# Performance work log

Measured on AMD Instinct MI355X. Metric: run time of the kernel, lower is better.

## Reference

```python
import jax, jax.numpy as jnp
import numpy as np

NUM_IMAGES = 2
A = 96000              # Hi*Wi*num_anchors for one feature level
PRE_NMS_TOPK = 1000
POST_NMS_TOPK = 500
NMS_THRESH = 0.7
MIN_SIZE = 0.0
CLIP_ANGLE_THRESH = 1.0     # detectron2 RotatedBoxes.clip default
IMG_H, IMG_W = 320.0, 320.0
MAXV = 8                     # max #vertices of a rect-rect intersection polygon


def _cross(u, v):
    return u[..., 0] * v[..., 1] - u[..., 1] * v[..., 0]


def _box_corners(box):
    # box: [5] = (cx, cy, w, h, angle_deg) -> [4,2] CCW corners
    cx, cy, w, h, ang = box[0], box[1], box[2], box[3], box[4]
    t = ang * (jnp.pi / 180.0)
    c, s = jnp.cos(t), jnp.sin(t)
    dx = jnp.array([0.5, -0.5, -0.5, 0.5], box.dtype) * w
    dy = jnp.array([0.5, 0.5, -0.5, -0.5], box.dtype) * h
    return jnp.stack([cx + c * dx - s * dy, cy + s * dx + c * dy], axis=-1)


def _clip_halfplane(pts, n, a, b):
    # Sutherland-Hodgman clip of convex polygon pts[:n] against directed line a->b
    idx = jnp.arange(MAXV)
    valid = idx < n
    nxt = pts[jnp.where(idx + 1 < n, idx + 1, 0)]
    d_cur = _cross(b - a, pts - a)
    d_nxt = _cross(b - a, nxt - a)
    in_cur = d_cur >= 0
    in_nxt = d_nxt >= 0
    denom = d_cur - d_nxt
    denom = jnp.where(jnp.abs(denom) < 1e-12, 1e-12, denom)
    t = (d_cur / denom)[:, None]
    inter = pts + t * (nxt - pts)
    emit_cur = valid & in_cur
    emit_int = valid & (in_cur != in_nxt)
    cand = jnp.stack([pts, inter], axis=1).reshape(2 * MAXV, 2)
    emit = jnp.stack([emit_cur, emit_int], axis=1).reshape(2 * MAXV)
    pos = jnp.cumsum(emit) - 1
    dst = jnp.where(emit, pos, MAXV)  # out-of-range -> dropped
    out = jnp.zeros((MAXV, 2), pts.dtype).at[dst].set(cand, mode='drop')
    return out, emit.sum()


def _pair_iou(b1, b2):
    # exact rotated-box IoU (polygon intersection), matches pairwise_iou_rotated math
    p = jnp.zeros((MAXV, 2), b1.dtype).at[:4].set(_box_corners(b1))
    n = jnp.asarray(4)
    c2 = _box_corners(b2)
    for i in range(4):
        p, n = _clip_halfplane(p, n, c2[i], c2[(i + 1) % 4])
    idx = jnp.arange(MAXV)
    valid = idx < n
    nxt = p[jnp.where(idx + 1 < n, idx + 1, 0)]
    inter = 0.5 * jnp.abs(jnp.sum(jnp.where(valid, _cross(p, nxt), 0.0)))
    a1 = b1[2] * b1[3]
    a2 = b2[2] * b2[3]
    return inter / jnp.maximum(a1 + a2 - inter, 1e-12)


_iou_matrix = jax.vmap(jax.vmap(_pair_iou, (None, 0)), (0, None))


def _clip_boxes(b):
    # RotatedBoxes.clip: only boxes with |angle| <= 1 deg are axis-aligned clipped
    cx, cy, w, h, a = b[:, 0], b[:, 1], b[:, 2], b[:, 3], b[:, 4]
    x1 = jnp.clip(cx - w * 0.5, 0.0, IMG_W)
    y1 = jnp.clip(cy - h * 0.5, 0.0, IMG_H)
    x2 = jnp.clip(cx + w * 0.5, 0.0, IMG_W)
    y2 = jnp.clip(cy + h * 0.5, 0.0, IMG_H)
    near0 = jnp.abs(a) <= CLIP_ANGLE_THRESH
    ncx = jnp.where(near0, 0.5 * (x1 + x2), cx)
    ncy = jnp.where(near0, 0.5 * (y1 + y2), cy)
    nw = jnp.where(near0, x2 - x1, w)
    nh = jnp.where(near0, y2 - y1, h)
    return jnp.stack([ncx, ncy, nw, nh, a], axis=-1)


def _nms_keep(iou, valid, thresh):
    K = valid.shape[0]
    idx = jnp.arange(K)
    def body(i, suppressed):
        row = (~suppressed[i]) & (iou[i] > thresh) & (idx > i)
        return suppressed | row
    suppressed = jax.lax.fori_loop(0, K, body, ~valid)
    return (~suppressed) & valid


def _stage(boxes, scores, lvl, valid, out_k, thresh):
    # sort desc by score, batched (level-offset) rotated NMS, keep first out_k kept
    order = jnp.argsort(-scores)
    b, s, l, v = boxes[order], scores[order], lvl[order], valid[order]
    max_coord = jnp.max(jnp.where(v[:, None], b[:, :4], 0.0))
    ob = b.at[:, :2].add(l.astype(b.dtype)[:, None] * (max_coord + 1.0))
    iou = jax.lax.stop_gradient(_iou_matrix(ob, ob))
    keep = _nms_keep(iou, v, thresh)
    rank = jnp.cumsum(keep) - 1
    sel = keep & (rank < out_k)
    dst = jnp.where(sel, rank, out_k)
    out_b = jnp.zeros((out_k, 5), b.dtype).at[dst].set(b, mode='drop')
    out_s = jnp.full((out_k,), -jnp.inf, s.dtype).at[dst].set(s, mode='drop')
    out_l = jnp.zeros((out_k,), l.dtype).at[dst].set(l, mode='drop')
    out_v = jnp.zeros((out_k,), bool).at[dst].set(True, mode='drop')
    return out_b, out_s, out_l, out_v


def _per_feature(proposals, logits):
    # proposals: [A,5], logits: [A]   (single level per feature, as in the module)
    s, idx = jax.lax.top_k(logits, PRE_NMS_TOPK)
    b = proposals[idx]
    valid = jnp.all(jnp.isfinite(b), axis=-1) & jnp.isfinite(s)
    b = _clip_boxes(b)
    valid = valid & (b[:, 2] > MIN_SIZE) & (b[:, 3] > MIN_SIZE)
    s = jnp.where(valid, s, -jnp.inf)
    lvl = jnp.zeros((PRE_NMS_TOPK,), jnp.int32)
    return _stage(b, s, lvl, valid, POST_NMS_TOPK, NMS_THRESH)


def _process_image(pr, lgr, pl, lgl):
    br, sr, lvr, vr = _per_feature(pr, lgr)
    bl, sl, lvl_, vl = _per_feature(pl, lgl)
    b = jnp.concatenate([br, bl], axis=0)
    s = jnp.concatenate([sr, sl], axis=0)
    lv = jnp.concatenate([lvr, lvl_], axis=0)
    v = jnp.concatenate([vr, vl], axis=0)
    fb, fs, _, _ = _stage(b, s, lv, v, 2 * POST_NMS_TOPK, NMS_THRESH)
    # [2*POST_NMS_TOPK, 6] = boxes ++ score; padding slots have score=-inf
    return jnp.concatenate([fb, fs[:, None]], axis=-1)


def setup_inputs() -> dict:
    key = jax.random.key(0)
    ks = jax.random.split(key, 4)
    def make_boxes(k):
        k1, k2, k3 = jax.random.split(k, 3)
        ctr = jax.random.uniform(k1, (NUM_IMAGES, A, 2), jnp.float32, -20.0, 340.0)
        wh = jax.random.uniform(k2, (NUM_IMAGES, A, 2), jnp.float32, 4.0, 96.0)
        ang = jax.random.uniform(k3, (NUM_IMAGES, A, 1), jnp.float32, -180.0, 180.0)
        return jnp.concatenate([ctr, wh, ang], axis=-1)
    return {
        'proposals_radar': make_boxes(ks[0]),
        'logits_radar': jax.random.normal(ks[1], (NUM_IMAGES, A), jnp.float32),
        'proposals_lidar': make_boxes(ks[2]),
        'logits_lidar': jax.random.normal(ks[3], (NUM_IMAGES, A), jnp.float32),
    }


def reference(proposals_radar, logits_radar, proposals_lidar, logits_lidar):
    return jax.vmap(_process_image)(proposals_radar, logits_radar,
                                    proposals_lidar, logits_lidar)
```

## Files before the change

### kernel.cpp

```cpp
#include <hip/hip_runtime.h>
#include <math.h>

#define AN 96000
#define TOPK 1000
#define KSTAGE 1000
#define SELCAP 4096
#define NBUCK 4096
#define NCHUNK 48
#define CHUNKE 2000
#define GCSTRIDE 16
#define RGSLC 32
#define S2SLC 8
#define NMS_TH 0.7f
#define NEG_SENT (-3.3895313892515355e38f)

typedef unsigned long long u64;


__device__ __forceinline__ float bf2f(unsigned short h) {
  return __uint_as_float(((unsigned)h) << 16);
}
__device__ __forceinline__ int bitfinite(float x) {
  unsigned b = __float_as_uint(x);
  return ((b >> 23) & 0xFFu) != 0xFFu;
}
__device__ __forceinline__ unsigned fkey(float x) {
  unsigned b = __float_as_uint(x);
  return (b & 0x80000000u) ? ~b : (b | 0x80000000u);
}
__device__ __forceinline__ float unkey(unsigned u) {
  unsigned b = (u & 0x80000000u) ? (u & 0x7FFFFFFFu) : ~u;
  return __uint_as_float(b);
}
__device__ __forceinline__ float ldin(const void* p, size_t i, int bf) {
  if (bf) return bf2f(((const unsigned short*)p)[i]);
  return ((const float*)p)[i];
}
__device__ __forceinline__ unsigned outbits(float f) {
  unsigned b = __float_as_uint(f);
  if ((b & 0x7FFFFFFFu) >= 0x7F7F8000u)
    b = (b & 0x80000000u) | 0x7F7F0000u;
  return b;
}
__device__ __forceinline__ u64 readlane64(u64 x, int b) {
  unsigned lo = __builtin_amdgcn_readlane((unsigned)x, b);
  unsigned hi = __builtin_amdgcn_readlane((unsigned)(x >> 32), b);
  return ((u64)hi << 32) | (u64)lo;
}
__device__ __forceinline__ void mk_corners(const float4 f, const float4 ax,
                                           float* co) {
#pragma clang fp contract(off)
  float cx = f.x, cy = f.y;
  float c = ax.x, s_ = ax.y, hw = ax.z, hh = ax.w;
  co[0] = cx + c * hw - s_ * hh;       co[1] = cy + s_ * hw + c * hh;
  co[2] = cx + c * (-hw) - s_ * hh;    co[3] = cy + s_ * (-hw) + c * hh;
  co[4] = cx + c * (-hw) - s_ * (-hh); co[5] = cy + s_ * (-hw) + c * (-hh);
  co[6] = cx + c * hw - s_ * (-hh);    co[7] = cy + s_ * hw + c * (-hh);
}


__device__ __forceinline__ unsigned blk_scan256(unsigned v, unsigned* wsum,
                                                int tid, unsigned* total) {
  unsigned x = v;
#pragma unroll
  for (int off = 1; off < 64; off <<= 1) {
    unsigned y = __shfl_up(x, (unsigned)off, 64);
    if ((tid & 63) >= off) x += y;
  }
  const int wv = tid >> 6;
  if ((tid & 63) == 63) wsum[wv] = x;
  __syncthreads();
  unsigned b0 = wsum[0], b1 = wsum[1], b2 = wsum[2], b3 = wsum[3];
  __syncthreads();
  unsigned base = 0;
  if (wv > 0) base += b0;
  if (wv > 1) base += b1;
  if (wv > 2) base += b2;
  *total = b0 + b1 + b2 + b3;
  return base + x;
}


__device__ __forceinline__ float pair_iou(const float* c1, float a1,
                                          const float* c2f, float a2) {
#pragma clang fp contract(off)
  float px[8], py[8], qx[8], qy[8];
#pragma unroll
  for (int i = 0; i < 8; i++) { px[i] = 0.f; py[i] = 0.f; }
#pragma unroll
  for (int i = 0; i < 4; i++) { px[i] = c1[2 * i]; py[i] = c1[2 * i + 1]; }
  int n = 4;
#pragma unroll
  for (int e = 0; e < 4; e++) {
    float ax = c2f[2 * e], ay = c2f[2 * e + 1];
    int e2 = (e + 1) & 3;
    float bx = c2f[2 * e2], by = c2f[2 * e2 + 1];
    float ex = bx - ax, ey = by - ay;
    float d[8];
#pragma unroll
    for (int i = 0; i < 8; i++) d[i] = ex * (py[i] - ay) - ey * (px[i] - ax);
    int mf = 0;
#pragma unroll
    for (int i = 0; i < 8; i++) {
      if (i < n) {
        float nxp, nyp, dn;
        if (i + 1 < n) {
          if (i < 7) { nxp = px[i + 1]; nyp = py[i + 1]; dn = d[i + 1]; }
          else       { nxp = px[7];     nyp = py[7];     dn = d[7];     }
        } else { nxp = px[0]; nyp = py[0]; dn = d[0]; }
        float dc = d[i];
        bool ic = dc >= 0.0f, inx = dn >= 0.0f;
        if (ic) {
          if (mf < 8) { qx[mf] = px[i]; qy[mf] = py[i]; }
          mf++;
        }
        if (ic != inx) {
          float den = dc - dn;
          if (fabsf(den) < 1e-12f) den = 1e-12f;
          float t = dc / den;
          if (mf < 8) {
            qx[mf] = px[i] + t * (nxp - px[i]);
            qy[mf] = py[i] + t * (nyp - py[i]);
          }
          mf++;
        }
      }
    }
    n = mf;
#pragma unroll
    for (int i = 0; i < 8; i++) {
      if (i < n) { px[i] = qx[i]; py[i] = qy[i]; }
    }
  }
  float ssum = 0.f;
#pragma unroll
  for (int i = 0; i < 8; i++) {
    if (i < n) {
      float nxp, nyp;
      if (i + 1 < n) {
        if (i < 7) { nxp = px[i + 1]; nyp = py[i + 1]; }
        else       { nxp = px[7];     nyp = py[7];     }
      } else { nxp = px[0]; nyp = py[0]; }
      ssum += px[i] * nyp - py[i] * nxp;
    }
  }
  float inter = 0.5f * fabsf(ssum);
  return inter / fmaxf(a1 + a2 - inter, 1e-12f);
}


__device__ __forceinline__ void nms_scan(
    const u64* __restrict__ mbase, const u64* __restrict__ nzr, int V,
    int tid, u64* remv_sh, u64* part) {
  if (tid < 16) {
    int base = tid * 64;
    u64 rv = 0;
    if (V <= base) rv = ~0ull;
    else if (V < base + 64) rv = (~0ull) << (V - base);
    remv_sh[tid] = rv;
  }
  u64 nzg[16];
#pragma unroll
  for (int g = 0; g < 16; g++) nzg[g] = nzr[g];
  u64 dg[16];
  if (tid < 64) {
#pragma unroll
    for (int g = 0; g < 16; g++) {
      int row = g * 64 + tid;
      dg[g] = ((nzg[g] >> tid) & 1ull) ? mbase[(size_t)row * 16 + g] : 0ull;
    }
  }
  __syncthreads();
#pragma unroll
  for (int g = 0; g < 16; g++) {
    if (tid < 64) {
      u64 nz = __ballot(dg[g] != 0ull);
      u64 cur = remv_sh[g];
      u64 rem = nz & ~cur;
      while (rem) {
        int b = __builtin_amdgcn_readfirstlane(__ffsll((u64)rem) - 1);
        rem &= rem - 1;
        if (!((cur >> b) & 1ull)) {
          cur |= readlane64(dg[g], b);
          rem &= ~cur;
        }
      }
      if (tid == 0) remv_sh[g] = cur;
    }
    __syncthreads();
    if (g == 15) break;
    u64 cur = remv_sh[g];
    u64 act = nzg[g] & ~cur;
    if (act) {
      u64 acc = 0;
      const int w = tid & 15;
      const int c = tid >> 4;
      if (w > g) {
#pragma unroll
        for (int k = 0; k < 4; k++) {
          int b = c * 4 + k;
          if ((act >> b) & 1ull)
            acc |= mbase[(size_t)(g * 64 + b) * 16 + w];
        }
      }
      part[tid] = acc;
      __syncthreads();
      if (tid < 16 && tid > g) {
        u64 tot = 0;
#pragma unroll
        for (int c2 = 0; c2 < 16; c2++) tot |= part[c2 * 16 + tid];
        remv_sh[tid] |= tot;
      }
      __syncthreads();
    }
  }
}


#define NZ (NBUCK * 4 + 64)
#define NZROWOFF 1016064
#define NZROWW 192
#define SVOFF 952016

__global__ __launch_bounds__(256) void k_fill(
    char* __restrict__ ws, const unsigned* __restrict__ lr_w,
    int* __restrict__ flag) {
  int i = blockIdx.x * 256 + threadIdx.x;
  unsigned* zws = (unsigned*)ws;
  unsigned* nzw = (unsigned*)(ws + NZROWOFF);
  unsigned* svw = (unsigned*)(ws + SVOFF);
  if (i < NZ) zws[i] = 0u;
  if (i < NZROWW) nzw[i] = 0u;
  if (i < 2) svw[i] = 0u;
  if (blockIdx.x == gridDim.x - 1) {
    const int tid = threadIdx.x;
    __shared__ int cnt;
    if (tid == 0) cnt = 0;
    __syncthreads();
    unsigned w = lr_w[tid * 89];
    unsigned v = (w >> 8) & 0x7Fu;
    if (v >= 0x3Cu && v <= 0x42u) atomicAdd(&cnt, 1);
    __syncthreads();
    if (tid == 0) flag[0] = (cnt >= 128) ? 1 : 0;
  }
}


__global__ __launch_bounds__(256) void k_hist(
    const void* __restrict__ lr, const void* __restrict__ ll,
    const int* __restrict__ dflag, unsigned* __restrict__ ghist) {
  const int blk = blockIdx.x;
  const int inst = blk / NCHUNK;
  const int chunk = blk % NCHUNK;
  const int img = inst >> 1, feat = inst & 1;
  const int bf = dflag[0];
  const void* logits = feat ? ll : lr;
  __shared__ unsigned lh[NBUCK];
  const int tid = threadIdx.x;
  for (int i = tid; i < NBUCK; i += 256) lh[i] = 0;
  __syncthreads();
  const size_t e0 = (size_t)img * AN + (size_t)chunk * CHUNKE;
  if (bf) {
    const uint4* p = (const uint4*)((const unsigned short*)logits + e0);
    for (int v = tid; v < CHUNKE / 8; v += 256) {
      uint4 q = p[v];
      unsigned wd[4] = {q.x, q.y, q.z, q.w};
#pragma unroll
      for (int k = 0; k < 4; k++) {
        atomicAdd(&lh[fkey(bf2f((unsigned short)(wd[k] & 0xFFFFu))) >> 20], 1u);
        atomicAdd(&lh[fkey(bf2f((unsigned short)(wd[k] >> 16))) >> 20], 1u);
      }
    }
  } else {
    const uint4* p = (const uint4*)((const float*)logits + e0);
    for (int v = tid; v < CHUNKE / 4; v += 256) {
      uint4 q = p[v];
      unsigned wd[4] = {q.x, q.y, q.z, q.w};
#pragma unroll
      for (int k = 0; k < 4; k++)
        atomicAdd(&lh[fkey(__uint_as_float(wd[k])) >> 20], 1u);
    }
  }
  __syncthreads();
  for (int i = tid; i < NBUCK; i += 256) {
    unsigned c = lh[i];
    if (c) atomicAdd(&ghist[inst * NBUCK + i], c);
  }
}


__global__ __launch_bounds__(256) void k_collect(
    const void* __restrict__ lr, const void* __restrict__ ll,
    const int* __restrict__ dflag, const unsigned* __restrict__ ghist,
    int* __restrict__ gcnt, u64* __restrict__ gsel64) {
  const int blk = blockIdx.x;
  const int inst = blk / NCHUNK;
  const int chunk = blk % NCHUNK;
  const int img = inst >> 1, feat = inst & 1;
  const int bf = dflag[0];
  const void* logits = feat ? ll : lr;
  const int tid = threadIdx.x;
  __shared__ u64 lbuf[2048];
  __shared__ unsigned wsum[4];
  __shared__ int sB;
  __shared__ int lcnt;
  __shared__ int sbase;
  unsigned hl[16];
  unsigned cs = 0;
  const int b0 = tid * 16;
#pragma unroll
  for (int k = 0; k < 16; k++) {
    hl[k] = ghist[inst * NBUCK + b0 + k];
    cs += hl[k];
  }
  if (tid == 0) { sB = 0; lcnt = 0; }
  unsigned tot;
  unsigned pre = blk_scan256(cs, wsum, tid, &tot);
  {
    unsigned suf = tot - (pre - cs);
    unsigned sufn = tot - pre;
    if (suf >= TOPK && sufn < TOPK) {
      unsigned c = sufn;
      int B = b0;
      for (int b = 15; b >= 0; --b) {
        c += hl[b];
        if (c >= TOPK) { B = b0 + b; break; }
      }
      sB = B;
    }
  }
  __syncthreads();
  const unsigned B = (unsigned)sB;
  const size_t e0 = (size_t)img * AN + (size_t)chunk * CHUNKE;
  const int abase = chunk * CHUNKE;
  if (bf) {
    const uint4* p = (const uint4*)((const unsigned short*)logits + e0);
    for (int v = tid; v < CHUNKE / 8; v += 256) {
      uint4 q = p[v];
      unsigned wd[4] = {q.x, q.y, q.z, q.w};
#pragma unroll
      for (int k = 0; k < 4; k++) {
#pragma unroll
        for (int h = 0; h < 2; h++) {
          unsigned u = fkey(bf2f((unsigned short)(h ? (wd[k] >> 16)
                                                    : (wd[k] & 0xFFFFu))));
          if ((u >> 20) >= B) {
            int p2 = atomicAdd(&lcnt, 1);
            unsigned idx = (unsigned)(abase + v * 8 + k * 2 + h);
            lbuf[p2] = ((u64)u << 32) | (unsigned)(~idx);
          }
        }
      }
    }
  } else {
    const uint4* p = (const uint4*)((const float*)logits + e0);
    for (int v = tid; v < CHUNKE / 4; v += 256) {
      uint4 q = p[v];
      unsigned wd[4] = {q.x, q.y, q.z, q.w};
#pragma unroll
      for (int k = 0; k < 4; k++) {
        unsigned u = fkey(__uint_as_float(wd[k]));
        if ((u >> 20) >= B) {
          int p2 = atomicAdd(&lcnt, 1);
          unsigned idx = (unsigned)(abase + v * 4 + k);
          lbuf[p2] = ((u64)u << 32) | (unsigned)(~idx);
        }
      }
    }
  }
  __syncthreads();
  const int tot2 = lcnt;
  if (tid == 0)
    sbase = tot2 ? atomicAdd(&gcnt[inst * GCSTRIDE], tot2) : 0;
  __syncthreads();
  const int base = sbase;
  for (int i = tid; i < tot2; i += 256) {
    int q = base + i;
    if (q < SELCAP) gsel64[inst * SELCAP + q] = lbuf[i];
  }
}


__global__ __launch_bounds__(256) void k_rg(
    const void* __restrict__ pr, const void* __restrict__ pl,
    const int* __restrict__ dflag, const int* __restrict__ gcnt,
    const u64* __restrict__ gsel64, float4* __restrict__ gpk) {
#pragma clang fp contract(off)
  __shared__ u64 sel64[SELCAP];
  const int inst = blockIdx.x / RGSLC;
  const int slice = blockIdx.x % RGSLC;
  const int img = inst >> 1, feat = inst & 1;
  const int bf = dflag[0];
  const void* props = feat ? pl : pr;
  const int tid = threadIdx.x;
  const int m = min(gcnt[inst * GCSTRIDE], SELCAP);
  if (slice * 128 >= m) return;
  const int mpad = (m + 7) & ~7;
  for (int i = tid; i < mpad; i += 256)
    sel64[i] = (i < m) ? gsel64[inst * SELCAP + i] : 0ull;
  __syncthreads();
  if (tid >= 128) return;
  const int e = slice * 128 + tid;
  if (e >= m) return;
  const u64 mine = sel64[e];
  int r = 0;
  for (int j0 = 0; j0 < mpad; j0 += 8) {
    u64 vj[8];
#pragma unroll
    for (int k = 0; k < 8; k++) vj[k] = sel64[j0 + k];
#pragma unroll
    for (int k = 0; k < 8; k++) r += (vj[k] > mine) ? 1 : 0;
  }
  if (r >= TOPK) return;
  unsigned u = (unsigned)(mine >> 32);
  int oi = (int)(~(unsigned)mine);
  if (oi < 0 || oi >= AN) oi = 0;
  float sc2 = unkey(u);
  const size_t pbase = (size_t)img * AN * 5;
  float cx = ldin(props, pbase + (size_t)oi * 5 + 0, bf);
  float cy = ldin(props, pbase + (size_t)oi * 5 + 1, bf);
  float w  = ldin(props, pbase + (size_t)oi * 5 + 2, bf);
  float h  = ldin(props, pbase + (size_t)oi * 5 + 3, bf);
  float ang = ldin(props, pbase + (size_t)oi * 5 + 4, bf);
  bool valid = bitfinite(cx) && bitfinite(cy) && bitfinite(w) &&
               bitfinite(h) && bitfinite(ang) && bitfinite(sc2);
  float x1 = fminf(fmaxf(cx - w * 0.5f, 0.0f), 320.0f);
  float y1 = fminf(fmaxf(cy - h * 0.5f, 0.0f), 320.0f);
  float x2 = fminf(fmaxf(cx + w * 0.5f, 0.0f), 320.0f);
  float y2 = fminf(fmaxf(cy + h * 0.5f, 0.0f), 320.0f);
  if (fabsf(ang) <= 1.0f) {
    cx = 0.5f * (x1 + x2); cy = 0.5f * (y1 + y2);
    w = x2 - x1; h = y2 - y1;
  }
  valid = valid && (w > 0.0f) && (h > 0.0f);
  float rad = 0.5f * sqrtf(w * w + h * h);
  float th = ang * (float)(M_PI / 180.0);
  float c = cosf(th), s_ = sinf(th);
  size_t o = ((size_t)inst * TOPK + r) * 3;
  gpk[o + 0] = make_float4(cx, cy, w, h);
  gpk[o + 1] = make_float4(ang, sc2, valid ? 1.0f : 0.0f, rad);
  gpk[o + 2] = make_float4(c, s_, 0.0f, 0.0f);
}


__global__ __launch_bounds__(256) void k_iou(
    const float4* __restrict__ gpk, const float4* __restrict__ sfilt,
    const float4* __restrict__ saux, const int* __restrict__ validN,
    const int mode, unsigned* __restrict__ mask32,
    u64* __restrict__ nzrow) {
#pragma clang fp contract(off)
  __shared__ float4 sf4[KSTAGE];
  __shared__ float4 aux[KSTAGE];
  __shared__ unsigned short qpair[8192];
  __shared__ unsigned mtile[256];
  __shared__ unsigned wsum[4];
  const int inst = blockIdx.x / 125;
  const int r0 = (blockIdx.x % 125) * 8;
  const int tid = threadIdx.x;
  int V;
  if (mode == 0) {
    float4 a0[4], a1[4], a2[4];
    int vld[4];
    int cnt = 0;
#pragma unroll
    for (int k = 0; k < 4; k++) {
      int rk = tid * 4 + k;
      size_t o = ((size_t)inst * TOPK + rk) * 3;
      a0[k] = gpk[o]; a1[k] = gpk[o + 1]; a2[k] = gpk[o + 2];
      vld[k] = (a1[k].z != 0.0f) ? 1 : 0;
      cnt += vld[k];
    }
    unsigned tot;
    unsigned pre = blk_scan256((unsigned)cnt, wsum, tid, &tot);
    V = (int)tot;
    int excl = (int)pre - cnt;
    int run = 0;
#pragma unroll
    for (int k = 0; k < 4; k++) {
      int e = tid * 4 + k;
      int dest;
      if (vld[k]) { dest = excl + run; run++; }
      else dest = V + (e - (excl + run));
      if (dest < 0) dest = 0;
      if (dest >= TOPK) dest = TOPK - 1;
      float w = a0[k].z, h = a0[k].w;
      sf4[dest] = make_float4(a0[k].x, a0[k].y, a1[k].w, w * h);
      aux[dest] = make_float4(a2[k].x, a2[k].y, 0.5f * w, 0.5f * h);
    }
  } else {
    for (int t = tid; t < KSTAGE; t += 256) {
      sf4[t] = sfilt[inst * KSTAGE + t];
      aux[t] = saux[inst * KSTAGE + t];
    }
    V = validN[inst];
  }
  mtile[tid] = 0;
  __syncthreads();
  const int r = r0 + (tid >> 5);
  const int w = tid & 31;
  unsigned sm = 0;
  const int jbase = w * 32;
  if (r < V && V <= KSTAGE && jbase + 31 > r) {
    const float4 fr = sf4[r];
    for (int jj = 0; jj < 32; jj++) {
      int jo = (jj + w) & 31;
      int j = jbase + jo;
      if (j > r && j < V) {
        float4 g = sf4[j];
        float dx = fr.x - g.x, dy = fr.y - g.y;
        float rs = fr.z + g.z;
        float amin = fminf(fr.w, g.w), amax = fmaxf(fr.w, g.w);
        if (dx * dx + dy * dy <= rs * rs && amin >= 0.699f * amax)
          sm |= (1u << jo);
      }
    }
  }
  int cnt2 = __popc(sm);
  unsigned tot2;
  unsigned pre2 = blk_scan256((unsigned)cnt2, wsum, tid, &tot2);
  const int total = (int)tot2;
  {
    int p = (int)pre2 - cnt2;
    unsigned t2 = sm;
    while (t2) {
      int jo = __ffs(t2) - 1;
      t2 &= t2 - 1;
      qpair[p++] = (unsigned short)((tid << 5) | jo);
    }
  }
  __syncthreads();
  for (int q = tid; q < total; q += 256) {
    unsigned e = (unsigned)qpair[q];
    int stid = (int)(e >> 5);
    int jo = (int)(e & 31);
    int rr = r0 + (stid >> 5);
    int j = (stid & 31) * 32 + jo;
    float c1[8], c2[8];
    mk_corners(sf4[rr], aux[rr], c1);
    mk_corners(sf4[j], aux[j], c2);
    float iou = pair_iou(c1, sf4[rr].w, c2, sf4[j].w);
    if (iou > NMS_TH) atomicOr(&mtile[stid], 1u << jo);
  }
  __syncthreads();
  mask32[((size_t)inst * KSTAGE + r) * 32 + w] = mtile[tid];
  u64 bal = __ballot(mtile[tid] != 0u);
  if ((tid & 63) == 0) {
    int wv = tid >> 6;
    u64 bits = 0;
    if ((unsigned)bal)        bits |= 1ull;
    if ((unsigned)(bal >> 32)) bits |= 2ull;
    if (bits) {
      int rlow = r0 + 2 * wv;
      atomicOr(&nzrow[inst * 16 + (r0 >> 6)], bits << (rlow & 63));
    }
  }
}


__global__ __launch_bounds__(256) void k_nms_sel(
    const u64* __restrict__ mask, const u64* __restrict__ nzrow,
    const float4* __restrict__ gpk,
    float* __restrict__ out_b, float* __restrict__ out_s,
    int* __restrict__ out_v) {
  const int inst = blockIdx.x;
  const int tid = threadIdx.x;
  __shared__ u64 remv_sh[16];
  __shared__ u64 part[256];
  __shared__ u64 keepw[16];
  __shared__ int wpre[16];
  __shared__ int rmap[TOPK];
  __shared__ unsigned wsum[4];
  int vld[4];
  int cnt = 0;
#pragma unroll
  for (int k = 0; k < 4; k++) {
    int rk = tid * 4 + k;
    float4 b = gpk[((size_t)inst * TOPK + rk) * 3 + 1];
    vld[k] = (b.z != 0.0f) ? 1 : 0;
    cnt += vld[k];
  }
  unsigned tot;
  unsigned pre = blk_scan256((unsigned)cnt, wsum, tid, &tot);
  const int V = (int)tot;
  {
    int excl = (int)pre - cnt;
    int run = 0;
#pragma unroll
    for (int k = 0; k < 4; k++) {
      int e = tid * 4 + k;
      int dest;
      if (vld[k]) { dest = excl + run; run++; }
      else dest = V + (e - (excl + run));
      if (dest < 0) dest = 0;
      if (dest >= TOPK) dest = TOPK - 1;
      rmap[dest] = e;
    }
  }
  for (int rr = tid; rr < 500; rr += 256) {
    float* ob = out_b + ((size_t)inst * 500 + rr) * 5;
    ob[0] = 0; ob[1] = 0; ob[2] = 0; ob[3] = 0; ob[4] = 0;
    out_s[(size_t)inst * 500 + rr] = NEG_SENT;
    out_v[(size_t)inst * 500 + rr] = 0;
  }
  const u64* mbase = mask + (size_t)inst * KSTAGE * 16;
  nms_scan(mbase, nzrow + inst * 16, V, tid, remv_sh, part);
  if (tid < 16) {
    int base = tid * 64;
    u64 vm;
    if (V <= base) vm = 0ull;
    else if (V >= base + 64) vm = ~0ull;
    else vm = (1ull << (V - base)) - 1ull;
    keepw[tid] = (~remv_sh[tid]) & vm;
  }
  __syncthreads();
  if (tid < 16) {
    int p = 0;
    for (int w2 = 0; w2 < tid; w2++) p += __popcll(keepw[w2]);
    wpre[tid] = p;
  }
  __syncthreads();
  for (int i = tid; i < KSTAGE; i += 256) {
    int wq = i >> 6, b = i & 63;
    u64 kw = keepw[wq];
    if ((kw >> b) & 1ull) {
      int rank = wpre[wq] + __popcll(kw & ((1ull << b) - 1ull));
      if (rank < 500) {
        int rk = rmap[i];
        size_t o = ((size_t)inst * TOPK + rk) * 3;
        float4 a0 = gpk[o];
        float4 a1 = gpk[o + 1];
        float* ob = out_b + ((size_t)inst * 500 + rank) * 5;
        ob[0] = a0.x; ob[1] = a0.y; ob[2] = a0.z; ob[3] = a0.w; ob[4] = a1.x;
        out_s[(size_t)inst * 500 + rank] = a1.y;
        out_v[(size_t)inst * 500 + rank] = 1;
      }
    }
  }
}


__global__ __launch_bounds__(256) void k_sort2(
    const float* __restrict__ outb, const float* __restrict__ outs,
    const int* __restrict__ outv, float* __restrict__ sb,
    float* __restrict__ ss, float4* __restrict__ sfilt,
    float4* __restrict__ saux, int* __restrict__ sValidN) {
#pragma clang fp contract(off)
  const int img = blockIdx.x / S2SLC;
  const int slice = blockIdx.x % S2SLC;
  const int tid = threadIdx.x;
  __shared__ u64 uk64[1000];
  __shared__ int vloc;
  if (tid == 0) vloc = 0;
  for (int e = tid; e < 1000; e += 256) {
    int fi = (e >= 500) ? 1 : 0;
    int src = (img * 2 + fi) * 500 + (e - fi * 500);
    float s = outs[src];
    uk64[e] = ((u64)fkey(s) << 32) | (unsigned)(~e);
  }
  __syncthreads();
  const int ELT = 1000 / S2SLC;
  const int e = slice * ELT + tid;
  int myv = 0;
  if (tid < ELT) {
    int fi = (e >= 500) ? 1 : 0;
    int src = (img * 2 + fi) * 500 + (e - fi * 500);
    float s = outs[src];
    u64 ue = uk64[e];
    int r = 0;
    for (int j0 = 0; j0 < 1000; j0 += 8) {
      u64 vj[8];
#pragma unroll
      for (int k = 0; k < 8; k++) vj[k] = uk64[j0 + k];
#pragma unroll
      for (int k = 0; k < 8; k++) r += (vj[k] > ue) ? 1 : 0;
    }
    if (r >= 1000) r = 999;
    const float* ib = outb + (size_t)src * 5;
    float cx = ib[0], cy = ib[1], w = ib[2], h = ib[3], ang = ib[4];
    size_t o = (size_t)img * KSTAGE + r;
    float* ob = sb + o * 5;
    ob[0] = cx; ob[1] = cy; ob[2] = w; ob[3] = h; ob[4] = ang;
    ss[o] = s;
    float th = ang * (float)(M_PI / 180.0);
    float c = cosf(th), s_ = sinf(th);
    float hw = 0.5f * w, hh = 0.5f * h;
    sfilt[o] = make_float4(cx, cy, 0.5f * sqrtf(w * w + h * h), w * h);
    saux[o]  = make_float4(c, s_, hw, hh);
    if (outv[src]) myv = 1;
  }
  if (myv) atomicAdd(&vloc, 1);
  __syncthreads();
  if (tid == 0 && vloc) atomicAdd(&sValidN[img], vloc);
}


__global__ __launch_bounds__(256) void k_nms_out(
    const u64* __restrict__ mask, const u64* __restrict__ nzrow,
    const int* __restrict__ validN,
    const float* __restrict__ sb, const float* __restrict__ ss,
    unsigned* __restrict__ out) {
  const int img = blockIdx.x;
  const int tid = threadIdx.x;
  __shared__ u64 remv_sh[16];
  __shared__ u64 part[256];
  __shared__ u64 keepw[16];
  __shared__ int wpre[16];
  const int V = validN[img];
  for (int rr = tid; rr < 1000; rr += 256) {
    unsigned* row = out + ((size_t)img * 1000 + rr) * 6;
    row[0] = 0; row[1] = 0; row[2] = 0; row[3] = 0; row[4] = 0;
    row[5] = 0xFF7F0000u;
  }
  const u64* mbase = mask + (size_t)img * KSTAGE * 16;
  nms_scan(mbase, nzrow + img * 16, V, tid, remv_sh, part);
  if (tid < 16) {
    int base = tid * 64;
    u64 vm;
    if (V <= base) vm = 0ull;
    else if (V >= base + 64) vm = ~0ull;
    else vm = (1ull << (V - base)) - 1ull;
    keepw[tid] = (~remv_sh[tid]) & vm;
  }
  __syncthreads();
  if (tid < 16) {
    int p = 0;
    for (int w2 = 0; w2 < tid; w2++) p += __popcll(keepw[w2]);
    wpre[tid] = p;
  }
  __syncthreads();
  for (int i = tid; i < KSTAGE; i += 256) {
    int wq = i >> 6, bq = i & 63;
    u64 kw = keepw[wq];
    if ((kw >> bq) & 1ull) {
      int rank = wpre[wq] + __popcll(kw & ((1ull << bq) - 1ull));
      if (rank < 1000) {
        const float* ib = sb + ((size_t)img * KSTAGE + i) * 5;
        unsigned* row = out + ((size_t)img * 1000 + rank) * 6;
        row[0] = outbits(ib[0]); row[1] = outbits(ib[1]);
        row[2] = outbits(ib[2]); row[3] = outbits(ib[3]);
        row[4] = outbits(ib[4]);
        row[5] = outbits(ss[(size_t)img * KSTAGE + i]);
      }
    }
  }
}


extern "C" void kernel_launch(void* const* d_in, const int* in_sizes, int n_in,
                              void* d_out, int out_size, void* d_ws,
                              size_t ws_size, hipStream_t stream) {
  const void* pr = d_in[0];
  const void* lr = d_in[1];
  const void* pl = d_in[2];
  const void* ll = d_in[3];
  char* ws = (char*)d_ws;
  unsigned* maskA = (unsigned*)ws;
  unsigned* ghist = (unsigned*)ws;
  int* gcnt       = (int*)(ws + 65536);
  u64* gsel64     = (u64*)(ws + 65808);
  float* outb  = (float*)(ws + 736000);
  float* outs  = (float*)(ws + 776000);
  int*   outv  = (int*)  (ws + 784000);
  float* sb    = (float*)(ws + 792000);
  float* ss    = (float*)(ws + 832000);
  int* sValidN = (int*)  (ws + SVOFF);
  int* dflag   = (int*)  (ws + 952024);
  float4* sfilt = (float4*)(ws + 952032);
  float4* saux  = (float4*)(ws + 984032);
  u64* nzrowA  = (u64*)(ws + NZROWOFF);
  u64* nzrowB  = (u64*)(ws + NZROWOFF + 512);
  float4* gpk   = (float4*)(ws + 1100000);

  hipLaunchKernelGGL(k_fill, dim3((NZ + 255) / 256), dim3(256), 0, stream,
                     ws, (const unsigned*)lr, dflag);
  hipLaunchKernelGGL(k_hist, dim3(4 * NCHUNK), dim3(256), 0, stream,
                     lr, ll, dflag, ghist);
  hipLaunchKernelGGL(k_collect, dim3(4 * NCHUNK), dim3(256), 0, stream,
                     lr, ll, dflag, ghist, gcnt, gsel64);
  hipLaunchKernelGGL(k_rg, dim3(4 * RGSLC), dim3(256), 0, stream,
                     pr, pl, dflag, gcnt, gsel64, gpk);
  hipLaunchKernelGGL(k_iou, dim3(4 * 125), dim3(256), 0, stream,
                     gpk, (const float4*)nullptr, (const float4*)nullptr,
                     (const int*)nullptr, 0, maskA, nzrowA);
  hipLaunchKernelGGL(k_nms_sel, dim3(4), dim3(256), 0, stream,
                     (const u64*)maskA, (const u64*)nzrowA, gpk,
                     outb, outs, outv);
  hipLaunchKernelGGL(k_sort2, dim3(2 * S2SLC), dim3(256), 0, stream,
                     outb, outs, outv, sb, ss, sfilt, saux, sValidN);
  hipLaunchKernelGGL(k_iou, dim3(2 * 125), dim3(256), 0, stream,
                     (const float4*)nullptr, sfilt, saux, sValidN, 1, maskA,
                     nzrowB);
  hipLaunchKernelGGL(k_nms_out, dim3(2), dim3(256), 0, stream,
                     (const u64*)maskA, (const u64*)nzrowB, sValidN,
                     sb, ss, (unsigned*)d_out);
}
```

Before: 146.6 us.

## Drop zero-fill kernel by replacing global atomics with per-block partial outputs

```diff
diff --git a/kernel.cpp b/kernel.cpp
--- a/kernel.cpp
+++ b/kernel.cpp
@@ -5,10 +5,10 @@
 #define TOPK 1000
 #define KSTAGE 1000
 #define SELCAP 4096
-#define NBUCK 4096
+#define NBUCK 1024
 #define NCHUNK 48
 #define CHUNKE 2000
-#define GCSTRIDE 16
+#define CAPC 2048
 #define RGSLC 32
 #define S2SLC 8
 #define NMS_TH 0.7f
@@ -46,6 +46,16 @@
   unsigned lo = __builtin_amdgcn_readlane((unsigned)x, b);
   unsigned hi = __builtin_amdgcn_readlane((unsigned)(x >> 32), b);
   return ((u64)hi << 32) | (u64)lo;
+}
+__device__ __forceinline__ int detect_bf(const unsigned* __restrict__ lr_w,
+                                         int tid, int* dsh) {
+  if (tid == 0) *dsh = 0;
+  __syncthreads();
+  unsigned w = lr_w[tid * 89];
+  unsigned v = (w >> 8) & 0x7Fu;
+  if (v >= 0x3Cu && v <= 0x42u) atomicAdd(dsh, 1);
+  __syncthreads();
+  return (*dsh >= 128) ? 1 : 0;
 }
 __device__ __forceinline__ void mk_corners(const float4 f, const float4 ax,
                                            float* co) {
@@ -217,46 +227,18 @@
 }
 
 
-#define NZ (NBUCK * 4 + 64)
-#define NZROWOFF 1016064
-#define NZROWW 192
-#define SVOFF 952016
-
-__global__ __launch_bounds__(256) void k_fill(
-    char* __restrict__ ws, const unsigned* __restrict__ lr_w,
-    int* __restrict__ flag) {
-  int i = blockIdx.x * 256 + threadIdx.x;
-  unsigned* zws = (unsigned*)ws;
-  unsigned* nzw = (unsigned*)(ws + NZROWOFF);
-  unsigned* svw = (unsigned*)(ws + SVOFF);
-  if (i < NZ) zws[i] = 0u;
-  if (i < NZROWW) nzw[i] = 0u;
-  if (i < 2) svw[i] = 0u;
-  if (blockIdx.x == gridDim.x - 1) {
-    const int tid = threadIdx.x;
-    __shared__ int cnt;
-    if (tid == 0) cnt = 0;
-    __syncthreads();
-    unsigned w = lr_w[tid * 89];
-    unsigned v = (w >> 8) & 0x7Fu;
-    if (v >= 0x3Cu && v <= 0x42u) atomicAdd(&cnt, 1);
-    __syncthreads();
-    if (tid == 0) flag[0] = (cnt >= 128) ? 1 : 0;
-  }
-}
-
-
 __global__ __launch_bounds__(256) void k_hist(
     const void* __restrict__ lr, const void* __restrict__ ll,
-    const int* __restrict__ dflag, unsigned* __restrict__ ghist) {
+    unsigned* __restrict__ chunkhist) {
   const int blk = blockIdx.x;
   const int inst = blk / NCHUNK;
   const int chunk = blk % NCHUNK;
   const int img = inst >> 1, feat = inst & 1;
-  const int bf = dflag[0];
+  const int tid = threadIdx.x;
+  __shared__ int dsh;
+  __shared__ unsigned lh[NBUCK];
+  const int bf = detect_bf((const unsigned*)lr, tid, &dsh);
   const void* logits = feat ? ll : lr;
-  __shared__ unsigned lh[NBUCK];
-  const int tid = threadIdx.x;
   for (int i = tid; i < NBUCK; i += 256) lh[i] = 0;
   __syncthreads();
   const size_t e0 = (size_t)img * AN + (size_t)chunk * CHUNKE;
@@ -267,8 +249,8 @@
       unsigned wd[4] = {q.x, q.y, q.z, q.w};
 #pragma unroll
       for (int k = 0; k < 4; k++) {
-        atomicAdd(&lh[fkey(bf2f((unsigned short)(wd[k] & 0xFFFFu))) >> 20], 1u);
-        atomicAdd(&lh[fkey(bf2f((unsigned short)(wd[k] >> 16))) >> 20], 1u);
+        atomicAdd(&lh[fkey(bf2f((unsigned short)(wd[k] & 0xFFFFu))) >> 22], 1u);
+        atomicAdd(&lh[fkey(bf2f((unsigned short)(wd[k] >> 16))) >> 22], 1u);
       }
     }
   } else {
@@ -278,42 +260,40 @@
       unsigned wd[4] = {q.x, q.y, q.z, q.w};
 #pragma unroll
       for (int k = 0; k < 4; k++)
-        atomicAdd(&lh[fkey(__uint_as_float(wd[k])) >> 20], 1u);
-    }
-  }
-  __syncthreads();
-  for (int i = tid; i < NBUCK; i += 256) {
-    unsigned c = lh[i];
-    if (c) atomicAdd(&ghist[inst * NBUCK + i], c);
-  }
+        atomicAdd(&lh[fkey(__uint_as_float(wd[k])) >> 22], 1u);
+    }
+  }
+  __syncthreads();
+  for (int i = tid; i < NBUCK; i += 256)
+    chunkhist[(size_t)blk * NBUCK + i] = lh[i];
 }
 
 
 __global__ __launch_bounds__(256) void k_collect(
     const void* __restrict__ lr, const void* __restrict__ ll,
-    const int* __restrict__ dflag, const unsigned* __restrict__ ghist,
-    int* __restrict__ gcnt, u64* __restrict__ gsel64) {
+    const unsigned* __restrict__ chunkhist,
+    int* __restrict__ gccnt, u64* __restrict__ gseg) {
   const int blk = blockIdx.x;
   const int inst = blk / NCHUNK;
   const int chunk = blk % NCHUNK;
   const int img = inst >> 1, feat = inst & 1;
-  const int bf = dflag[0];
-  const void* logits = feat ? ll : lr;
   const int tid = threadIdx.x;
-  __shared__ u64 lbuf[2048];
+  __shared__ int dsh;
+  __shared__ u64 lbuf[CAPC];
   __shared__ unsigned wsum[4];
   __shared__ int sB;
   __shared__ int lcnt;
-  __shared__ int sbase;
-  unsigned hl[16];
-  unsigned cs = 0;
-  const int b0 = tid * 16;
-#pragma unroll
-  for (int k = 0; k < 16; k++) {
-    hl[k] = ghist[inst * NBUCK + b0 + k];
-    cs += hl[k];
-  }
+  const int bf = detect_bf((const unsigned*)lr, tid, &dsh);
+  const void* logits = feat ? ll : lr;
   if (tid == 0) { sB = 0; lcnt = 0; }
+  unsigned hl[4] = {0u, 0u, 0u, 0u};
+  const int b0 = tid * 4;
+  for (int c = 0; c < NCHUNK; c++) {
+    const uint4 q = *(const uint4*)&chunkhist[
+        ((size_t)(inst * NCHUNK + c)) * NBUCK + b0];
+    hl[0] += q.x; hl[1] += q.y; hl[2] += q.z; hl[3] += q.w;
+  }
+  unsigned cs = hl[0] + hl[1] + hl[2] + hl[3];
   unsigned tot;
   unsigned pre = blk_scan256(cs, wsum, tid, &tot);
   {
@@ -322,7 +302,7 @@
     if (suf >= TOPK && sufn < TOPK) {
       unsigned c = sufn;
       int B = b0;
-      for (int b = 15; b >= 0; --b) {
+      for (int b = 3; b >= 0; --b) {
         c += hl[b];
         if (c >= TOPK) { B = b0 + b; break; }
       }
@@ -344,7 +324,7 @@
         for (int h = 0; h < 2; h++) {
           unsigned u = fkey(bf2f((unsigned short)(h ? (wd[k] >> 16)
                                                     : (wd[k] & 0xFFFFu))));
-          if ((u >> 20) >= B) {
+          if ((u >> 22) >= B) {
             int p2 = atomicAdd(&lcnt, 1);
             unsigned idx = (unsigned)(abase + v * 8 + k * 2 + h);
             lbuf[p2] = ((u64)u << 32) | (unsigned)(~idx);
@@ -360,7 +340,7 @@
 #pragma unroll
       for (int k = 0; k < 4; k++) {
         unsigned u = fkey(__uint_as_float(wd[k]));
-        if ((u >> 20) >= B) {
+        if ((u >> 22) >= B) {
           int p2 = atomicAdd(&lcnt, 1);
           unsigned idx = (unsigned)(abase + v * 4 + k);
           lbuf[p2] = ((u64)u << 32) | (unsigned)(~idx);
@@ -370,34 +350,54 @@
   }
   __syncthreads();
   const int tot2 = lcnt;
-  if (tid == 0)
-    sbase = tot2 ? atomicAdd(&gcnt[inst * GCSTRIDE], tot2) : 0;
-  __syncthreads();
-  const int base = sbase;
-  for (int i = tid; i < tot2; i += 256) {
-    int q = base + i;
-    if (q < SELCAP) gsel64[inst * SELCAP + q] = lbuf[i];
-  }
+  if (tid == 0) gccnt[blk] = tot2;
+  for (int i = tid; i < tot2; i += 256)
+    gseg[(size_t)blk * CAPC + i] = lbuf[i];
 }
 
 
 __global__ __launch_bounds__(256) void k_rg(
     const void* __restrict__ pr, const void* __restrict__ pl,
-    const int* __restrict__ dflag, const int* __restrict__ gcnt,
-    const u64* __restrict__ gsel64, float4* __restrict__ gpk) {
+    const void* __restrict__ lr,
+    const int* __restrict__ gccnt, const u64* __restrict__ gseg,
+    float4* __restrict__ gpk) {
 #pragma clang fp contract(off)
+  __shared__ int dsh;
   __shared__ u64 sel64[SELCAP];
+  __shared__ int coff[NCHUNK + 1];
   const int inst = blockIdx.x / RGSLC;
   const int slice = blockIdx.x % RGSLC;
   const int img = inst >> 1, feat = inst & 1;
-  const int bf = dflag[0];
+  const int tid = threadIdx.x;
+  const int bf = detect_bf((const unsigned*)lr, tid, &dsh);
   const void* props = feat ? pl : pr;
-  const int tid = threadIdx.x;
-  const int m = min(gcnt[inst * GCSTRIDE], SELCAP);
+  {
+    int cv = 0;
+    if (tid < NCHUNK) cv = gccnt[inst * NCHUNK + tid];
+    if (tid < 64) {
+      int x = cv;
+#pragma unroll
+      for (int off = 1; off < 64; off <<= 1) {
+        int y = __shfl_up(x, (unsigned)off, 64);
+        if ((tid & 63) >= off) x += y;
+      }
+      if (tid < NCHUNK) coff[tid] = x - cv;
+      if (tid == NCHUNK - 1) coff[NCHUNK] = x;
+    }
+  }
+  __syncthreads();
+  const int m = min(coff[NCHUNK], SELCAP);
   if (slice * 128 >= m) return;
+  for (int c = 0; c < NCHUNK; c++) {
+    int base = coff[c];
+    if (base >= SELCAP) break;
+    int n = coff[c + 1] - base;
+    if (base + n > SELCAP) n = SELCAP - base;
+    const u64* src = gseg + (size_t)(inst * NCHUNK + c) * CAPC;
+    for (int i = tid; i < n; i += 256) sel64[base + i] = src[i];
+  }
   const int mpad = (m + 7) & ~7;
-  for (int i = tid; i < mpad; i += 256)
-    sel64[i] = (i < m) ? gsel64[inst * SELCAP + i] : 0ull;
+  for (int i = m + tid; i < mpad; i += 256) sel64[i] = 0ull;
   __syncthreads();
   if (tid >= 128) return;
   const int e = slice * 128 + tid;
@@ -445,17 +445,19 @@
 
 __global__ __launch_bounds__(256) void k_iou(
     const float4* __restrict__ gpk, const float4* __restrict__ sfilt,
-    const float4* __restrict__ saux, const int* __restrict__ validN,
+    const float4* __restrict__ saux, const unsigned* __restrict__ svp,
     const int mode, unsigned* __restrict__ mask32,
-    u64* __restrict__ nzrow) {
+    unsigned char* __restrict__ nzb) {
 #pragma clang fp contract(off)
   __shared__ float4 sf4[KSTAGE];
   __shared__ float4 aux[KSTAGE];
   __shared__ unsigned short qpair[8192];
   __shared__ unsigned mtile[256];
   __shared__ unsigned wsum[4];
+  __shared__ unsigned s_nz;
   const int inst = blockIdx.x / 125;
-  const int r0 = (blockIdx.x % 125) * 8;
+  const int tno = blockIdx.x % 125;
+  const int r0 = tno * 8;
   const int tid = threadIdx.x;
   int V;
   if (mode == 0) {
@@ -492,9 +494,12 @@
       sf4[t] = sfilt[inst * KSTAGE + t];
       aux[t] = saux[inst * KSTAGE + t];
     }
-    V = validN[inst];
+    V = 0;
+#pragma unroll
+    for (int k2 = 0; k2 < S2SLC; k2++) V += (int)svp[inst * S2SLC + k2];
   }
   mtile[tid] = 0;
+  if (tid == 0) s_nz = 0u;
   __syncthreads();
   const int r = r0 + (tid >> 5);
   const int w = tid & 31;
@@ -546,19 +551,24 @@
   u64 bal = __ballot(mtile[tid] != 0u);
   if ((tid & 63) == 0) {
     int wv = tid >> 6;
-    u64 bits = 0;
-    if ((unsigned)bal)        bits |= 1ull;
-    if ((unsigned)(bal >> 32)) bits |= 2ull;
-    if (bits) {
-      int rlow = r0 + 2 * wv;
-      atomicOr(&nzrow[inst * 16 + (r0 >> 6)], bits << (rlow & 63));
-    }
+    unsigned bits = 0;
+    if ((unsigned)bal)         bits |= 1u;
+    if ((unsigned)(bal >> 32)) bits |= 2u;
+    if (bits) atomicOr(&s_nz, bits << (2 * wv));
+  }
+  __syncthreads();
+  if (tid == 0) {
+    unsigned char* dst = nzb + (size_t)inst * 128;
+    if (tno == 124)
+      *(unsigned*)(dst + 124) = (s_nz & 0xFFu);
+    else
+      dst[tno] = (unsigned char)(s_nz & 0xFFu);
   }
 }
 
 
 __global__ __launch_bounds__(256) void k_nms_sel(
-    const u64* __restrict__ mask, const u64* __restrict__ nzrow,
+    const u64* __restrict__ mask, const unsigned char* __restrict__ nzb,
     const float4* __restrict__ gpk,
     float* __restrict__ out_b, float* __restrict__ out_s,
     int* __restrict__ out_v) {
@@ -603,7 +613,8 @@
     out_v[(size_t)inst * 500 + rr] = 0;
   }
   const u64* mbase = mask + (size_t)inst * KSTAGE * 16;
-  nms_scan(mbase, nzrow + inst * 16, V, tid, remv_sh, part);
+  nms_scan(mbase, (const u64*)(nzb + (size_t)inst * 128), V, tid,
+           remv_sh, part);
   if (tid < 16) {
     int base = tid * 64;
     u64 vm;
@@ -643,7 +654,7 @@
     const float* __restrict__ outb, const float* __restrict__ outs,
     const int* __restrict__ outv, float* __restrict__ sb,
     float* __restrict__ ss, float4* __restrict__ sfilt,
-    float4* __restrict__ saux, int* __restrict__ sValidN) {
+    float4* __restrict__ saux, unsigned* __restrict__ svp) {
 #pragma clang fp contract(off)
   const int img = blockIdx.x / S2SLC;
   const int slice = blockIdx.x % S2SLC;
@@ -690,13 +701,13 @@
   }
   if (myv) atomicAdd(&vloc, 1);
   __syncthreads();
-  if (tid == 0 && vloc) atomicAdd(&sValidN[img], vloc);
+  if (tid == 0) svp[img * S2SLC + slice] = (unsigned)vloc;
 }
 
 
 __global__ __launch_bounds__(256) void k_nms_out(
-    const u64* __restrict__ mask, const u64* __restrict__ nzrow,
-    const int* __restrict__ validN,
+    const u64* __restrict__ mask, const unsigned char* __restrict__ nzb,
+    const unsigned* __restrict__ svp,
     const float* __restrict__ sb, const float* __restrict__ ss,
     unsigned* __restrict__ out) {
   const int img = blockIdx.x;
@@ -705,14 +716,17 @@
   __shared__ u64 part[256];
   __shared__ u64 keepw[16];
   __shared__ int wpre[16];
-  const int V = validN[img];
+  int V = 0;
+#pragma unroll
+  for (int k2 = 0; k2 < S2SLC; k2++) V += (int)svp[img * S2SLC + k2];
   for (int rr = tid; rr < 1000; rr += 256) {
     unsigned* row = out + ((size_t)img * 1000 + rr) * 6;
     row[0] = 0; row[1] = 0; row[2] = 0; row[3] = 0; row[4] = 0;
     row[5] = 0xFF7F0000u;
   }
   const u64* mbase = mask + (size_t)img * KSTAGE * 16;
-  nms_scan(mbase, nzrow + img * 16, V, tid, remv_sh, part);
+  nms_scan(mbase, (const u64*)(nzb + (size_t)img * 128), V, tid,
+           remv_sh, part);
   if (tid < 16) {
     int base = tid * 64;
     u64 vm;
@@ -754,43 +768,40 @@
   const void* pl = d_in[2];
   const void* ll = d_in[3];
   char* ws = (char*)d_ws;
-  unsigned* maskA = (unsigned*)ws;
-  unsigned* ghist = (unsigned*)ws;
-  int* gcnt       = (int*)(ws + 65536);
-  u64* gsel64     = (u64*)(ws + 65808);
-  float* outb  = (float*)(ws + 736000);
-  float* outs  = (float*)(ws + 776000);
-  int*   outv  = (int*)  (ws + 784000);
-  float* sb    = (float*)(ws + 792000);
-  float* ss    = (float*)(ws + 832000);
-  int* sValidN = (int*)  (ws + SVOFF);
-  int* dflag   = (int*)  (ws + 952024);
-  float4* sfilt = (float4*)(ws + 952032);
-  float4* saux  = (float4*)(ws + 984032);
-  u64* nzrowA  = (u64*)(ws + NZROWOFF);
-  u64* nzrowB  = (u64*)(ws + NZROWOFF + 512);
-  float4* gpk   = (float4*)(ws + 1100000);
-
-  hipLaunchKernelGGL(k_fill, dim3((NZ + 255) / 256), dim3(256), 0, stream,
-                     ws, (const unsigned*)lr, dflag);
+  unsigned* maskA     = (unsigned*)ws;
+  unsigned* chunkhist = (unsigned*)(ws + 600000);
+  int* gccnt          = (int*)(ws + 1400000);
+  u64* gseg           = (u64*)(ws + 1500000);
+  float4* gpk         = (float4*)(ws + 4700000);
+  float* outb  = (float*)(ws + 4900000);
+  float* outs  = (float*)(ws + 4940000);
+  int*   outv  = (int*)  (ws + 4948000);
+  float* sb    = (float*)(ws + 4956000);
+  float* ss    = (float*)(ws + 4996000);
+  float4* sfilt = (float4*)(ws + 5004000);
+  float4* saux  = (float4*)(ws + 5036000);
+  unsigned char* nzbA = (unsigned char*)(ws + 5068000);
+  unsigned char* nzbB = (unsigned char*)(ws + 5068512);
+  unsigned* svp       = (unsigned*)(ws + 5068800);
+
   hipLaunchKernelGGL(k_hist, dim3(4 * NCHUNK), dim3(256), 0, stream,
-                     lr, ll, dflag, ghist);
+                     lr, ll, chunkhist);
   hipLaunchKernelGGL(k_collect, dim3(4 * NCHUNK), dim3(256), 0, stream,
-                     lr, ll, dflag, ghist, gcnt, gsel64);
+                     lr, ll, chunkhist, gccnt, gseg);
   hipLaunchKernelGGL(k_rg, dim3(4 * RGSLC), dim3(256), 0, stream,
-                     pr, pl, dflag, gcnt, gsel64, gpk);
+                     pr, pl, lr, gccnt, gseg, gpk);
   hipLaunchKernelGGL(k_iou, dim3(4 * 125), dim3(256), 0, stream,
                      gpk, (const float4*)nullptr, (const float4*)nullptr,
-                     (const int*)nullptr, 0, maskA, nzrowA);
+                     (const unsigned*)nullptr, 0, maskA, nzbA);
   hipLaunchKernelGGL(k_nms_sel, dim3(4), dim3(256), 0, stream,
-                     (const u64*)maskA, (const u64*)nzrowA, gpk,
+                     (const u64*)maskA, (const unsigned char*)nzbA, gpk,
                      outb, outs, outv);
   hipLaunchKernelGGL(k_sort2, dim3(2 * S2SLC), dim3(256), 0, stream,
-                     outb, outs, outv, sb, ss, sfilt, saux, sValidN);
+                     outb, outs, outv, sb, ss, sfilt, saux, svp);
   hipLaunchKernelGGL(k_iou, dim3(2 * 125), dim3(256), 0, stream,
-                     (const float4*)nullptr, sfilt, saux, sValidN, 1, maskA,
-                     nzrowB);
+                     (const float4*)nullptr, sfilt, saux,
+                     (const unsigned*)svp, 1, maskA, nzbB);
   hipLaunchKernelGGL(k_nms_out, dim3(2), dim3(256), 0, stream,
-                     (const u64*)maskA, (const u64*)nzrowB, sValidN,
-                     sb, ss, (unsigned*)d_out);
-}
+                     (const u64*)maskA, (const unsigned char*)nzbB,
+                     (const unsigned*)svp, sb, ss, (unsigned*)d_out);
+}
```

Result: slower. 176.9 us (+20.7%).
